# Kernel tuning notes

Hardware: AMD Instinct MI355X
Metric: run time of the kernel (lower is better)

Reference implementation:

```python
import jax, jax.numpy as jnp
import numpy as np

EPS = 1e-12
LAMBDA = 0.5  # kernel['lambda'] for the binary kernel

D, H, Z = 3072, 1024, 32
BS, NN = 128, 32


def setup_inputs() -> dict:
    key = jax.random.key(0)
    ks = jax.random.split(key, 16)
    sc = lambda fan_in: 1.0 / np.sqrt(fan_in)
    inp = {
        "x_c": jax.random.normal(ks[0], (BS, D), jnp.float32),
        "x_nn": jax.random.normal(ks[1], (BS, NN, D), jnp.float32),
        # encoder params: D -> H -> H -> Z
        "We1": jax.random.normal(ks[2], (D, H), jnp.float32) * sc(D),
        "be1": jnp.zeros((H,), jnp.float32),
        "We2": jax.random.normal(ks[3], (H, H), jnp.float32) * sc(H),
        "be2": jnp.zeros((H,), jnp.float32),
        "We3": jax.random.normal(ks[4], (H, Z), jnp.float32) * sc(H),
        "be3": jnp.zeros((Z,), jnp.float32),
        # decoder params: Z -> H -> H -> D
        "Wd1": jax.random.normal(ks[5], (Z, H), jnp.float32) * sc(Z),
        "bd1": jnp.zeros((H,), jnp.float32),
        "Wd2": jax.random.normal(ks[6], (H, H), jnp.float32) * sc(H),
        "bd2": jnp.zeros((H,), jnp.float32),
        "Wd3": jax.random.normal(ks[7], (H, D), jnp.float32) * sc(H),
        "bd3": jnp.zeros((D,), jnp.float32),
    }
    return inp


def _mlp(x, W1, b1, W2, b2, W3, b3):
    h = jax.nn.relu(x @ W1 + b1)
    h = jax.nn.relu(h @ W2 + b2)
    return h @ W3 + b3


def reference(x_c, x_nn, We1, be1, We2, be2, We3, be3,
              Wd1, bd1, Wd2, bd2, Wd3, bd3):
    bs, num_nn, dim = x_nn.shape

    enc = lambda x: _mlp(x, We1, be1, We2, be2, We3, be3)
    dec = lambda z: _mlp(z, Wd1, bd1, Wd2, bd2, Wd3, bd3)

    z_c = enc(x_c)                                   # (bs, Z)
    z_dim = z_c.shape[1]
    z_nn = enc(x_nn.reshape(-1, dim)).reshape(bs, num_nn, z_dim)

    recon = dec(z_c)                                 # (bs, D)
    dz = z_nn - z_c[:, None, :]                      # (bs, nn, Z)
    v = dz.reshape(-1, z_dim)                        # (bs*nn, Z)
    inputs = jnp.broadcast_to(z_c[:, None, :], (bs, num_nn, z_dim)).reshape(-1, z_dim)

    # approx_order == 2: Jacobian-vector and Hessian-bilinear (dz^T H dz) via nested jvp
    jac_fn = lambda z: jax.jvp(dec, (z,), (v,))[1]   # J(z) dz, (bs*nn, D)
    jac, hess = jax.jvp(jac_fn, (inputs,), (v,))     # each (bs*nn, D)

    n_recon = recon[:, None, :] + (jac + 0.5 * hess).reshape(bs, num_nn, dim)

    n_loss = jnp.sum((x_nn - n_recon) ** 2, axis=2)  # ||.||^2, (bs, nn)

    # binary kernel: 1 where neighbor differs from center, lambda where identical
    dist = jnp.linalg.norm(x_c[:, None, :] - x_nn, axis=2)
    weights = jnp.where(dist > EPS, 1.0, LAMBDA)

    loss = jnp.mean(weights * n_loss)
    return loss
```

## Files before the change

kernel.cpp:

```cpp
#include <hip/hip_runtime.h>
#include <math.h>

#define D_DIM 3072
#define H_DIM 1024
#define Z_DIM 32
#define BATCH 128
#define NNEI 32
#define NROWS (BATCH * NNEI)
#define MENC (NROWS + BATCH)

typedef __attribute__((ext_vector_type(8))) short short8;
typedef __attribute__((ext_vector_type(4))) float f32x4;
typedef unsigned short ushortT;

__device__ __forceinline__ unsigned short f2bf(float f) {
  union { float f; unsigned int u; } v; v.f = f;
  unsigned int r = v.u + 0x7FFFu + ((v.u >> 16) & 1u);
  return (unsigned short)(r >> 16);
}
__device__ __forceinline__ float bf2f(unsigned short b) {
  union { unsigned int u; float f; } v; v.u = ((unsigned int)b) << 16;
  return v.f;
}

enum { EP_RELU = 0, EP_BIAS = 1, EP_PART = 2, EP_LOSS = 3 };

template <int MODE, int TN>
__global__ __launch_bounds__(256) __attribute__((amdgpu_waves_per_eu(2, 4)))
void gemm64(
    const ushortT* __restrict__ A, const ushortT* __restrict__ BT,
    const float* __restrict__ bias, ushortT* __restrict__ C,
    float* __restrict__ P, int M, int N, int K, int Ks,
    const ushortT* __restrict__ xa,
    const float* __restrict__ wrow,
    float* __restrict__ out) {
  constexpr int NF = TN / 32;

  __shared__ __align__(16) ushortT As[8192];
  __shared__ __align__(16) ushortT Bs[TN * 64];

  const int t = threadIdx.x;
  const int wave = t >> 6;
  const int lane = t & 63;
  const int quad = lane >> 4;
  const int lm = lane & 15;

  int id = blockIdx.y * gridDim.x + blockIdx.x;
  const int nwg = gridDim.x * gridDim.y;
  if ((nwg & 7) == 0) id = (id & 7) * (nwg >> 3) + (id >> 3);
  const int bm = (id / gridDim.x) * 128;
  const int bn = (id % gridDim.x) * TN;

  const int koff = blockIdx.z * Ks;
  const int wr = (wave >> 1) * 64;
  const int wc = (wave & 1) * (TN / 2);

  f32x4 acc[4][NF];
#pragma unroll
  for (int i = 0; i < 4; ++i)
#pragma unroll
    for (int j = 0; j < NF; ++j) acc[i][j] = (f32x4)0.f;

  const int a_r0 = (t >> 6) * 16 + (t & 15);
  const int a_q8 = ((t >> 4) & 3) * 8;
  const ushortT* ga = A + (size_t)(bm + a_r0) * K + koff + a_q8;
  const size_t aK64 = (size_t)64 * K;

  const ushortT* gb = nullptr;
  if (TN >= 64) {
    gb = BT + (size_t)(bn + a_r0) * K + koff + a_q8;
  } else {
    const int b_r = ((t >> 6) & 1) * 16 + (t & 15);
    const int b_k = (t >> 7) * 32 + ((t >> 4) & 3) * 8;
    gb = BT + (size_t)(bn + b_r) * K + koff + b_k;
  }

  uint4 a0, a1, a2, a3, b0, b1 = {0,0,0,0}, b2 = {0,0,0,0}, b3 = {0,0,0,0};

#define LOADT(kk)                                               \
  {                                                             \
    const size_t o = (size_t)(kk) * 64;                         \
    a0 = *(const uint4*)(ga + o);                               \
    a1 = *(const uint4*)(ga + aK64 + o);                        \
    a2 = *(const uint4*)(ga + o + 32);                          \
    a3 = *(const uint4*)(ga + aK64 + o + 32);                   \
    b0 = *(const uint4*)(gb + o);                               \
    if (TN == 128) {                                            \
      b1 = *(const uint4*)(gb + aK64 + o);                      \
      b2 = *(const uint4*)(gb + o + 32);                        \
      b3 = *(const uint4*)(gb + aK64 + o + 32);                 \
    } else if (TN == 64) {                                      \
      b1 = *(const uint4*)(gb + o + 32);                        \
    }                                                           \
  }
#define STORET()                                                \
  {                                                             \
    *(uint4*)&As[t * 8] = a0;                                   \
    *(uint4*)&As[t * 8 + 2048] = a1;                            \
    *(uint4*)&As[t * 8 + 4096] = a2;                            \
    *(uint4*)&As[t * 8 + 6144] = a3;                            \
    *(uint4*)&Bs[t * 8] = b0;                                   \
    if (TN == 128) {                                            \
      *(uint4*)&Bs[t * 8 + 2048] = b1;                          \
      *(uint4*)&Bs[t * 8 + 4096] = b2;                          \
      *(uint4*)&Bs[t * 8 + 6144] = b3;                          \
    } else if (TN == 64) {                                      \
      *(uint4*)&Bs[t * 8 + 2048] = b1;                          \
    }                                                           \
  }

  const int nk = Ks / 64;
  LOADT(0);

  for (int k0 = 0; k0 < nk; ++k0) {
    __syncthreads();
    STORET();
    __syncthreads();
    if (k0 + 1 < nk) LOADT(k0 + 1);

#pragma unroll
    for (int kk = 0; kk < 2; ++kk) {
      const ushortT* arp = &As[kk * 4096 + (wr >> 4) * 512 + lane * 8];
      const ushortT* brp =
          &Bs[(TN == 128 ? kk * 4096 : TN == 64 ? kk * 2048 : kk * 1024) +
              (wc >> 4) * 512 + lane * 8];
      short8 af[4], bf[NF];
#pragma unroll
      for (int mt = 0; mt < 4; ++mt) af[mt] = *(const short8*)(arp + mt * 512);
#pragma unroll
      for (int nt = 0; nt < NF; ++nt) bf[nt] = *(const short8*)(brp + nt * 512);
#pragma unroll
      for (int mt = 0; mt < 4; ++mt)
#pragma unroll
        for (int nt = 0; nt < NF; ++nt)
          acc[mt][nt] = __builtin_amdgcn_mfma_f32_16x16x32_bf16(af[mt], bf[nt], acc[mt][nt], 0, 0, 0);
    }
  }
#undef LOADT
#undef STORET

  if (MODE == EP_LOSS) {
    __shared__ float red[256];
    float lsum = 0.f;
#pragma unroll
    for (int mt = 0; mt < 4; ++mt) {
#pragma unroll
      for (int r = 0; r < 4; ++r) {
        const int row = bm + wr + mt * 16 + quad * 4 + r;
        const float w = wrow[row];
        const ushortT* xr = xa + (size_t)row * N;
        float rs = 0.f;
#pragma unroll
        for (int nt = 0; nt < NF; ++nt) {
          const int col = bn + wc + nt * 16 + lm;
          const float d = bf2f(xr[col]) - (acc[mt][nt][r] + bias[col]);
          rs = fmaf(d, d, rs);
        }
        lsum = fmaf(w, rs, lsum);
      }
    }
    __syncthreads();
    red[t] = lsum;
    __syncthreads();
    for (int st = 128; st > 0; st >>= 1) {
      if (t < st) red[t] += red[t + st];
      __syncthreads();
    }
    if (t == 0) atomicAdd(out, red[0] * (1.0f / (float)NROWS));
  } else if (MODE == EP_PART) {
#pragma unroll
    for (int mt = 0; mt < 4; ++mt)
#pragma unroll
      for (int r = 0; r < 4; ++r) {
        const int row = bm + wr + mt * 16 + quad * 4 + r;
#pragma unroll
        for (int nt = 0; nt < NF; ++nt) {
          const int col = bn + wc + nt * 16 + lm;
          P[((size_t)blockIdx.z * M + row) * N + col] = acc[mt][nt][r];
        }
      }
  } else {
#pragma unroll
    for (int mt = 0; mt < 4; ++mt)
#pragma unroll
      for (int r = 0; r < 4; ++r) {
        const int row = bm + wr + mt * 16 + quad * 4 + r;
#pragma unroll
        for (int nt = 0; nt < NF; ++nt) {
          const int col = bn + wc + nt * 16 + lm;
          float v = acc[mt][nt][r] + bias[col];
          if (MODE == EP_RELU) v = fmaxf(v, 0.f);
          C[(size_t)row * N + col] = f2bf(v);
        }
      }
  }
}

template <int MODE, int TN>
__global__ __launch_bounds__(256) __attribute__((amdgpu_waves_per_eu(2, 4)))
void gemm_sb(
    const ushortT* __restrict__ A, const ushortT* __restrict__ BT,
    const float* __restrict__ bias, ushortT* __restrict__ C,
    int M, int N, int K,
    const ushortT* __restrict__ xa, const float* __restrict__ wrow,
    float* __restrict__ out) {
  constexpr int NF = TN / 32;
  __shared__ __align__(16) ushortT As[4096];
  __shared__ __align__(16) ushortT Bs[TN * 32];

  const int t = threadIdx.x;
  const int wave = t >> 6;
  const int lane = t & 63;
  const int quad = lane >> 4;
  const int lm = lane & 15;

  int id = blockIdx.y * gridDim.x + blockIdx.x;
  const int nwg = gridDim.x * gridDim.y;
  if ((nwg & 7) == 0) id = (id & 7) * (nwg >> 3) + (id >> 3);
  const int bm = (id / gridDim.x) * 128;
  const int bn = (id % gridDim.x) * TN;

  const int wr = (wave >> 1) * 64;
  const int wc = (wave & 1) * (TN / 2);

  f32x4 acc[4][NF];
#pragma unroll
  for (int i = 0; i < 4; ++i)
#pragma unroll
    for (int j = 0; j < NF; ++j) acc[i][j] = (f32x4)0.f;

  const int a_r0 = (t >> 6) * 16 + (t & 15);
  const int a_q8 = ((t >> 4) & 3) * 8;
  const ushortT* ga0 = A + (size_t)(bm + a_r0) * K + a_q8;
  const ushortT* ga1 = ga0 + (size_t)64 * K;
  const ushortT* gb0 = BT + (size_t)(bn + a_r0) * K + a_q8;
  const ushortT* gb1 = gb0 + (size_t)64 * K;

  uint4 ra0 = *(const uint4*)ga0;
  uint4 ra1 = *(const uint4*)ga1;
  uint4 rb0 = *(const uint4*)gb0;
  uint4 rb1 = {0, 0, 0, 0};
  if (TN == 128) rb1 = *(const uint4*)gb1;
  ga0 += 32; ga1 += 32; gb0 += 32; gb1 += 32;

  const ushortT* arp = As + (wr >> 4) * 512 + lane * 8;
  const ushortT* brp = Bs + (wc >> 4) * 512 + lane * 8;

  for (int k0 = 0; k0 < K; k0 += 32) {
    __syncthreads();
    *(uint4*)&As[t * 8] = ra0;
    *(uint4*)&As[t * 8 + 2048] = ra1;
    *(uint4*)&Bs[t * 8] = rb0;
    if (TN == 128) *(uint4*)&Bs[t * 8 + 2048] = rb1;
    __syncthreads();
    if (k0 + 32 < K) {
      ra0 = *(const uint4*)ga0;
      ra1 = *(const uint4*)ga1;
      rb0 = *(const uint4*)gb0;
      if (TN == 128) rb1 = *(const uint4*)gb1;
      ga0 += 32; ga1 += 32; gb0 += 32; gb1 += 32;
    }
    short8 af[4], bf[NF];
#pragma unroll
    for (int mt = 0; mt < 4; ++mt) af[mt] = *(const short8*)(arp + mt * 512);
#pragma unroll
    for (int nt = 0; nt < NF; ++nt) bf[nt] = *(const short8*)(brp + nt * 512);
#pragma unroll
    for (int mt = 0; mt < 4; ++mt)
#pragma unroll
      for (int nt = 0; nt < NF; ++nt)
        acc[mt][nt] = __builtin_amdgcn_mfma_f32_16x16x32_bf16(af[mt], bf[nt], acc[mt][nt], 0, 0, 0);
  }

#pragma unroll
  for (int mt = 0; mt < 4; ++mt)
#pragma unroll
    for (int r = 0; r < 4; ++r) {
      const int row = bm + wr + mt * 16 + quad * 4 + r;
#pragma unroll
      for (int nt = 0; nt < NF; ++nt) {
        const int col = bn + wc + nt * 16 + lm;
        float v = acc[mt][nt][r] + bias[col];
        if (MODE == EP_RELU) v = fmaxf(v, 0.f);
        C[(size_t)row * N + col] = f2bf(v);
      }
    }
}

template <int S>
__global__ __launch_bounds__(256) void reduce_lin(
    const float* __restrict__ P, const float* __restrict__ bias,
    ushortT* __restrict__ outp, int MN, int Nmask) {
  const int i4 = (blockIdx.x * 256 + threadIdx.x) * 4;
  if (i4 >= MN) return;
  float4 s = *(const float4*)(P + i4);
#pragma unroll
  for (int k = 1; k < S; ++k) {
    const float4 q = *(const float4*)(P + (size_t)k * MN + i4);
    s.x += q.x; s.y += q.y; s.z += q.z; s.w += q.w;
  }
  const float4 b = *(const float4*)(bias + (i4 & Nmask));
  ushort4 o;
  o.x = f2bf(s.x + b.x); o.y = f2bf(s.y + b.y);
  o.z = f2bf(s.z + b.z); o.w = f2bf(s.w + b.w);
  *(ushort4*)(outp + i4) = o;
}

__global__ __launch_bounds__(256) void mask_apply(
    const ushortT* __restrict__ U, ushortT* __restrict__ outp) {
  const int i4 = (blockIdx.x * 256 + threadIdx.x) * 4;
  const int r = i4 >> 10;
  const int c = i4 & 1023;
  ushort4 u = *(const ushort4*)(U + i4);
  ushort4 o;
  if (r < NROWS) {
    const ushort4 m = *(const ushort4*)(U + (((size_t)(NROWS + (r >> 5))) << 10) + c);
    o.x = ((short)m.x > 0) ? u.x : 0;
    o.y = ((short)m.y > 0) ? u.y : 0;
    o.z = ((short)m.z > 0) ? u.z : 0;
    o.w = ((short)m.w > 0) ? u.w : 0;
  } else {
    o.x = ((short)u.x > 0) ? u.x : 0;
    o.y = ((short)u.y > 0) ? u.y : 0;
    o.z = ((short)u.z > 0) ? u.z : 0;
    o.w = ((short)u.w > 0) ? u.w : 0;
  }
  *(ushort4*)(outp + i4) = o;
}

__global__ __launch_bounds__(256) void prep_kernel(
    const float* __restrict__ x_c, const float* __restrict__ x_nn,
    ushortT* __restrict__ A_enc, float* __restrict__ wbuf, float* __restrict__ out) {
  const int i = blockIdx.x;
  const int t = threadIdx.x;
  if (i < NROWS) {
    const float* src = x_nn + (size_t)i * D_DIM;
    const float* ctr = x_c + (size_t)(i >> 5) * D_DIM;
    ushortT* dst = A_enc + (size_t)i * D_DIM;
    float s = 0.f;
    for (int d = t * 4; d < D_DIM; d += 1024) {
      const float4 v = *(const float4*)(src + d);
      const float4 c = *(const float4*)(ctr + d);
      ushort4 o;
      o.x = f2bf(v.x); o.y = f2bf(v.y); o.z = f2bf(v.z); o.w = f2bf(v.w);
      *(ushort4*)(dst + d) = o;
      const float dx = v.x - c.x, dy = v.y - c.y, dz = v.z - c.z, dw = v.w - c.w;
      s += dx * dx + dy * dy + dz * dz + dw * dw;
    }
    __shared__ float red[256];
    red[t] = s;
    __syncthreads();
    for (int st = 128; st > 0; st >>= 1) {
      if (t < st) red[t] += red[t + st];
      __syncthreads();
    }
    if (t == 0) {
      wbuf[i] = (red[0] > 1e-24f) ? 1.0f : 0.5f;
      if (i == 0) out[0] = 0.f;
    }
  } else {
    const int r = i - NROWS;
    const float* src = x_c + (size_t)r * D_DIM;
    ushortT* dst = A_enc + (size_t)i * D_DIM;
    for (int d = t * 4; d < D_DIM; d += 1024) {
      const float4 v = *(const float4*)(src + d);
      ushort4 o;
      o.x = f2bf(v.x); o.y = f2bf(v.y); o.z = f2bf(v.z); o.w = f2bf(v.w);
      *(ushort4*)(dst + d) = o;
    }
  }
}

__global__ __launch_bounds__(256) void trans_all(
    const float* __restrict__ We1, const float* __restrict__ We2,
    const float* __restrict__ We3, const float* __restrict__ Wd1,
    const float* __restrict__ Wd2, const float* __restrict__ Wd3,
    ushortT* __restrict__ We1T, ushortT* __restrict__ We2T,
    ushortT* __restrict__ We3T, ushortT* __restrict__ Wd1T,
    ushortT* __restrict__ Wd2T, ushortT* __restrict__ Wd3T) {
  const int b = blockIdx.x;
  const float* W; ushortT* WT; int K, N, loc;
  if (b < 3072)      { W = We1; WT = We1T; K = 3072; N = 1024; loc = b; }
  else if (b < 4096) { W = We2; WT = We2T; K = 1024; N = 1024; loc = b - 3072; }
  else if (b < 4128) { W = We3; WT = We3T; K = 1024; N = 32;   loc = b - 4096; }
  else if (b < 4160) { W = Wd1; WT = Wd1T; K = 32;   N = 1024; loc = b - 4128; }
  else if (b < 5184) { W = Wd2; WT = Wd2T; K = 1024; N = 1024; loc = b - 4160; }
  else               { W = Wd3; WT = Wd3T; K = 1024; N = 3072; loc = b - 5184; }
  const int ntiles = N >> 5;
  const int n0 = (loc % ntiles) * 32;
  const int k0 = (loc / ntiles) * 32;
  __shared__ float tile[32][33];
  const int tx = threadIdx.x & 31;
  const int ty = threadIdx.x >> 5;
  for (int i = ty; i < 32; i += 8)
    tile[i][tx] = W[(size_t)(k0 + i) * N + n0 + tx];
  __syncthreads();
  for (int i = ty; i < 32; i += 8)
    WT[(size_t)(n0 + i) * K + k0 + tx] = f2bf(tile[tx][i]);
}

extern "C" void kernel_launch(void* const* d_in, const int* in_sizes, int n_in,
                              void* d_out, int out_size, void* d_ws, size_t ws_size,
                              hipStream_t stream) {
  const float* x_c = (const float*)d_in[0];
  const float* x_nn = (const float*)d_in[1];
  const float* We1 = (const float*)d_in[2];
  const float* be1 = (const float*)d_in[3];
  const float* We2 = (const float*)d_in[4];
  const float* be2 = (const float*)d_in[5];
  const float* We3 = (const float*)d_in[6];
  const float* be3 = (const float*)d_in[7];
  const float* Wd1 = (const float*)d_in[8];
  const float* bd1 = (const float*)d_in[9];
  const float* Wd2 = (const float*)d_in[10];
  const float* bd2 = (const float*)d_in[11];
  const float* Wd3 = (const float*)d_in[12];
  const float* bd3 = (const float*)d_in[13];
  float* out = (float*)d_out;

  char* p = (char*)d_ws;
  auto alloc = [&](size_t bytes) {
    char* r = p;
    p += (bytes + 255) & ~(size_t)255;
    return r;
  };
  ushortT* We1T = (ushortT*)alloc((size_t)H_DIM * D_DIM * 2);
  ushortT* We2T = (ushortT*)alloc((size_t)H_DIM * H_DIM * 2);
  ushortT* We3T = (ushortT*)alloc((size_t)Z_DIM * H_DIM * 2);
  ushortT* Wd1T = (ushortT*)alloc((size_t)H_DIM * Z_DIM * 2);
  ushortT* Wd2T = (ushortT*)alloc((size_t)H_DIM * H_DIM * 2);
  ushortT* Wd3T = (ushortT*)alloc((size_t)D_DIM * H_DIM * 2);
  ushortT* A_enc = (ushortT*)alloc((size_t)MENC * D_DIM * 2);
  ushortT* bufX = (ushortT*)alloc((size_t)MENC * H_DIM * 2);
  ushortT* bufY = (ushortT*)alloc((size_t)MENC * H_DIM * 2);
  ushortT* z = (ushortT*)alloc((size_t)MENC * Z_DIM * 2);
  float* Pz = (float*)alloc((size_t)8 * MENC * Z_DIM * 4);
  float* wbuf = (float*)alloc((size_t)NROWS * 4);

  const dim3 blk(256);
  const float* nofp = nullptr;
  const ushortT* nobf = nullptr;

  prep_kernel<<<dim3(MENC), blk, 0, stream>>>(x_c, x_nn, A_enc, wbuf, out);
  trans_all<<<dim3(8256), blk, 0, stream>>>(We1, We2, We3, Wd1, Wd2, Wd3,
                                            We1T, We2T, We3T, Wd1T, Wd2T, Wd3T);

  gemm64<EP_RELU, 64><<<dim3(16, 33, 1), blk, 0, stream>>>(
      A_enc, We1T, be1, bufX, nullptr, MENC, H_DIM, D_DIM, D_DIM, nobf, nofp, nullptr);
  gemm64<EP_RELU, 64><<<dim3(16, 33, 1), blk, 0, stream>>>(
      bufX, We2T, be2, bufY, nullptr, MENC, H_DIM, H_DIM, H_DIM, nobf, nofp, nullptr);
  gemm64<EP_PART, 32><<<dim3(1, 33, 8), blk, 0, stream>>>(
      bufY, We3T, nofp, nullptr, Pz, MENC, Z_DIM, H_DIM, H_DIM / 8, nobf, nofp, nullptr);
  reduce_lin<8><<<dim3((MENC * Z_DIM) / 1024), blk, 0, stream>>>(
      Pz, be3, z, MENC * Z_DIM, Z_DIM - 1);

  gemm_sb<EP_BIAS, 64><<<dim3(16, 33), blk, 0, stream>>>(
      z, Wd1T, bd1, bufX, MENC, H_DIM, Z_DIM, nobf, nofp, nullptr);
  mask_apply<<<dim3((MENC * H_DIM) / 1024), blk, 0, stream>>>(bufX, bufY);
  gemm64<EP_BIAS, 64><<<dim3(16, 33, 1), blk, 0, stream>>>(
      bufY, Wd2T, bd2, bufX, nullptr, MENC, H_DIM, H_DIM, H_DIM, nobf, nofp, nullptr);
  mask_apply<<<dim3((NROWS * H_DIM) / 1024), blk, 0, stream>>>(bufX, bufY);
  gemm64<EP_LOSS, 128><<<dim3(24, 32, 1), blk, 0, stream>>>(
      bufY, Wd3T, bd3, nullptr, nullptr, NROWS, D_DIM, H_DIM, H_DIM, A_enc, wbuf, out);
}
```

Measured before the change: 410.2 us.

## Double-buffer GEMM tiles via direct global-to-LDS loads and widen N tiles

Replaces the register-staged global-load-then-LDS-store scheme in the GEMM kernels with global_load_lds direct copies into double-buffered shared memory, using vmcnt waits and raw barriers so the next K tile streams in while the current one is computed. The single-K-step small GEMM is simplified to one direct load plus compute. The encoder and decoder hidden GEMMs move from 64-wide to 128-wide N tiles, halving the grid, and the waves_per_eu hint is dropped. This aims to cut VGPR staging and LDS store overhead and to improve latency hiding, at the cost of doubled LDS use, which may lower occupancy, and a smaller grid.

Result: faster. 401.6 us (-2.1%).

```diff
diff --git a/kernel.cpp b/kernel.cpp
--- a/kernel.cpp
+++ b/kernel.cpp
@@ -23,11 +23,27 @@
   return v.f;
 }
 
+__device__ __forceinline__ void gl16(const ushortT* g, ushortT* l) {
+  typedef __attribute__((address_space(1))) const void gvoid;
+  typedef __attribute__((address_space(3))) void lvoid;
+  __builtin_amdgcn_global_load_lds((gvoid*)(const void*)g, (lvoid*)(void*)l,
+                                   16, 0, 0);
+}
+
+template <int N>
+__device__ __forceinline__ void wait_vmcnt() {
+  if constexpr (N == 0)      asm volatile("s_waitcnt vmcnt(0)" ::: "memory");
+  else if constexpr (N == 5) asm volatile("s_waitcnt vmcnt(5)" ::: "memory");
+  else if constexpr (N == 6) asm volatile("s_waitcnt vmcnt(6)" ::: "memory");
+  else if constexpr (N == 8) asm volatile("s_waitcnt vmcnt(8)" ::: "memory");
+}
+#define BAR() asm volatile("s_barrier" ::: "memory")
+#define LGKM0() asm volatile("s_waitcnt lgkmcnt(0)" ::: "memory")
+
 enum { EP_RELU = 0, EP_BIAS = 1, EP_PART = 2, EP_LOSS = 3 };
 
 template <int MODE, int TN>
-__global__ __launch_bounds__(256) __attribute__((amdgpu_waves_per_eu(2, 4)))
-void gemm64(
+__global__ __launch_bounds__(256) void gemm64(
     const ushortT* __restrict__ A, const ushortT* __restrict__ BT,
     const float* __restrict__ bias, ushortT* __restrict__ C,
     float* __restrict__ P, int M, int N, int K, int Ks,
@@ -35,9 +51,10 @@
     const float* __restrict__ wrow,
     float* __restrict__ out) {
   constexpr int NF = TN / 32;
-
-  __shared__ __align__(16) ushortT As[8192];
-  __shared__ __align__(16) ushortT Bs[TN * 64];
+  constexpr int NLD = 4 + NF;
+
+  __shared__ __align__(16) ushortT As[2][8192];
+  __shared__ __align__(16) ushortT Bs[2][TN * 64];
 
   const int t = threadIdx.x;
   const int wave = t >> 6;
@@ -66,7 +83,7 @@
   const ushortT* ga = A + (size_t)(bm + a_r0) * K + koff + a_q8;
   const size_t aK64 = (size_t)64 * K;
 
-  const ushortT* gb = nullptr;
+  const ushortT* gb;
   if (TN >= 64) {
     gb = BT + (size_t)(bn + a_r0) * K + koff + a_q8;
   } else {
@@ -75,69 +92,81 @@
     gb = BT + (size_t)(bn + b_r) * K + koff + b_k;
   }
 
-  uint4 a0, a1, a2, a3, b0, b1 = {0,0,0,0}, b2 = {0,0,0,0}, b3 = {0,0,0,0};
-
-#define LOADT(kk)                                               \
+  ushortT* asw0 = &As[0][wave * 512];
+  ushortT* asw1 = &As[1][wave * 512];
+  ushortT* bsw0 = &Bs[0][wave * 512];
+  ushortT* bsw1 = &Bs[1][wave * 512];
+
+#define STAGE(asw, bsw, kk)                                     \
   {                                                             \
     const size_t o = (size_t)(kk) * 64;                         \
-    a0 = *(const uint4*)(ga + o);                               \
-    a1 = *(const uint4*)(ga + aK64 + o);                        \
-    a2 = *(const uint4*)(ga + o + 32);                          \
-    a3 = *(const uint4*)(ga + aK64 + o + 32);                   \
-    b0 = *(const uint4*)(gb + o);                               \
+    gl16(ga + o, (asw));                                        \
+    gl16(ga + aK64 + o, (asw) + 2048);                          \
+    gl16(ga + o + 32, (asw) + 4096);                            \
+    gl16(ga + aK64 + o + 32, (asw) + 6144);                     \
+    gl16(gb + o, (bsw));                                        \
     if (TN == 128) {                                            \
-      b1 = *(const uint4*)(gb + aK64 + o);                      \
-      b2 = *(const uint4*)(gb + o + 32);                        \
-      b3 = *(const uint4*)(gb + aK64 + o + 32);                 \
+      gl16(gb + aK64 + o, (bsw) + 2048);                        \
+      gl16(gb + o + 32, (bsw) + 4096);                          \
+      gl16(gb + aK64 + o + 32, (bsw) + 6144);                   \
     } else if (TN == 64) {                                      \
-      b1 = *(const uint4*)(gb + o + 32);                        \
+      gl16(gb + o + 32, (bsw) + 2048);                          \
     }                                                           \
   }
-#define STORET()                                                \
-  {                                                             \
-    *(uint4*)&As[t * 8] = a0;                                   \
-    *(uint4*)&As[t * 8 + 2048] = a1;                            \
-    *(uint4*)&As[t * 8 + 4096] = a2;                            \
-    *(uint4*)&As[t * 8 + 6144] = a3;                            \
-    *(uint4*)&Bs[t * 8] = b0;                                   \
-    if (TN == 128) {                                            \
-      *(uint4*)&Bs[t * 8 + 2048] = b1;                          \
-      *(uint4*)&Bs[t * 8 + 4096] = b2;                          \
-      *(uint4*)&Bs[t * 8 + 6144] = b3;                          \
-    } else if (TN == 64) {                                      \
-      *(uint4*)&Bs[t * 8 + 2048] = b1;                          \
-    }                                                           \
+
+#define COMPUTE(b)                                                            \
+  {                                                                           \
+    _Pragma("unroll")                                                         \
+    for (int kk = 0; kk < 2; ++kk) {                                          \
+      const ushortT* arp = &As[b][kk * 4096 + (wr >> 4) * 512 + lane * 8];    \
+      const ushortT* brp =                                                    \
+          &Bs[b][(TN == 128 ? kk * 4096 : TN == 64 ? kk * 2048 : kk * 1024) + \
+                 (wc >> 4) * 512 + lane * 8];                                 \
+      short8 af[4], bf[NF];                                                   \
+      _Pragma("unroll")                                                       \
+      for (int mt = 0; mt < 4; ++mt)                                          \
+        af[mt] = *(const short8*)(arp + mt * 512);                            \
+      _Pragma("unroll")                                                       \
+      for (int nt = 0; nt < NF; ++nt)                                         \
+        bf[nt] = *(const short8*)(brp + nt * 512);                            \
+      _Pragma("unroll")                                                       \
+      for (int mt = 0; mt < 4; ++mt)                                          \
+        _Pragma("unroll")                                                     \
+        for (int nt = 0; nt < NF; ++nt)                                       \
+          acc[mt][nt] = __builtin_amdgcn_mfma_f32_16x16x32_bf16(              \
+              af[mt], bf[nt], acc[mt][nt], 0, 0, 0);                          \
+    }                                                                         \
   }
 
   const int nk = Ks / 64;
-  LOADT(0);
-
-  for (int k0 = 0; k0 < nk; ++k0) {
-    __syncthreads();
-    STORET();
-    __syncthreads();
-    if (k0 + 1 < nk) LOADT(k0 + 1);
-
-#pragma unroll
-    for (int kk = 0; kk < 2; ++kk) {
-      const ushortT* arp = &As[kk * 4096 + (wr >> 4) * 512 + lane * 8];
-      const ushortT* brp =
-          &Bs[(TN == 128 ? kk * 4096 : TN == 64 ? kk * 2048 : kk * 1024) +
-              (wc >> 4) * 512 + lane * 8];
-      short8 af[4], bf[NF];
-#pragma unroll
-      for (int mt = 0; mt < 4; ++mt) af[mt] = *(const short8*)(arp + mt * 512);
-#pragma unroll
-      for (int nt = 0; nt < NF; ++nt) bf[nt] = *(const short8*)(brp + nt * 512);
-#pragma unroll
-      for (int mt = 0; mt < 4; ++mt)
-#pragma unroll
-        for (int nt = 0; nt < NF; ++nt)
-          acc[mt][nt] = __builtin_amdgcn_mfma_f32_16x16x32_bf16(af[mt], bf[nt], acc[mt][nt], 0, 0, 0);
-    }
-  }
-#undef LOADT
-#undef STORET
+  STAGE(asw0, bsw0, 0);
+
+  for (int k0 = 0; k0 < nk; k0 += 2) {
+    BAR();
+    if (k0 + 1 < nk) {
+      STAGE(asw1, bsw1, k0 + 1);
+      wait_vmcnt<NLD>();
+    } else {
+      wait_vmcnt<0>();
+    }
+    BAR();
+    COMPUTE(0);
+    LGKM0();
+    if (k0 + 1 < nk) {
+      BAR();
+      if (k0 + 2 < nk) {
+        STAGE(asw0, bsw0, k0 + 2);
+        wait_vmcnt<NLD>();
+      } else {
+        wait_vmcnt<0>();
+      }
+      BAR();
+      COMPUTE(1);
+      LGKM0();
+    }
+  }
+#undef STAGE
+#undef COMPUTE
 
   if (MODE == EP_LOSS) {
     __shared__ float red[256];
@@ -197,8 +226,7 @@
 }
 
 template <int MODE, int TN>
-__global__ __launch_bounds__(256) __attribute__((amdgpu_waves_per_eu(2, 4)))
-void gemm_sb(
+__global__ __launch_bounds__(256) void gemm_sb(
     const ushortT* __restrict__ A, const ushortT* __restrict__ BT,
     const float* __restrict__ bias, ushortT* __restrict__ C,
     int M, int N, int K,
@@ -223,54 +251,39 @@
   const int wr = (wave >> 1) * 64;
   const int wc = (wave & 1) * (TN / 2);
 
-  f32x4 acc[4][NF];
-#pragma unroll
-  for (int i = 0; i < 4; ++i)
-#pragma unroll
-    for (int j = 0; j < NF; ++j) acc[i][j] = (f32x4)0.f;
-
   const int a_r0 = (t >> 6) * 16 + (t & 15);
   const int a_q8 = ((t >> 4) & 3) * 8;
   const ushortT* ga0 = A + (size_t)(bm + a_r0) * K + a_q8;
-  const ushortT* ga1 = ga0 + (size_t)64 * K;
   const ushortT* gb0 = BT + (size_t)(bn + a_r0) * K + a_q8;
-  const ushortT* gb1 = gb0 + (size_t)64 * K;
-
-  uint4 ra0 = *(const uint4*)ga0;
-  uint4 ra1 = *(const uint4*)ga1;
-  uint4 rb0 = *(const uint4*)gb0;
-  uint4 rb1 = {0, 0, 0, 0};
-  if (TN == 128) rb1 = *(const uint4*)gb1;
-  ga0 += 32; ga1 += 32; gb0 += 32; gb1 += 32;
+
+  ushortT* asw = &As[wave * 512];
+  ushortT* bsw = &Bs[wave * 512];
+  gl16(ga0, asw);
+  gl16(ga0 + (size_t)64 * K, asw + 2048);
+  gl16(gb0, bsw);
+  if (TN == 128) gl16(gb0 + (size_t)64 * K, bsw + 2048);
+  wait_vmcnt<0>();
+  BAR();
+
+  f32x4 acc[4][NF];
+#pragma unroll
+  for (int i = 0; i < 4; ++i)
+#pragma unroll
+    for (int j = 0; j < NF; ++j) acc[i][j] = (f32x4)0.f;
 
   const ushortT* arp = As + (wr >> 4) * 512 + lane * 8;
   const ushortT* brp = Bs + (wc >> 4) * 512 + lane * 8;
-
-  for (int k0 = 0; k0 < K; k0 += 32) {
-    __syncthreads();
-    *(uint4*)&As[t * 8] = ra0;
-    *(uint4*)&As[t * 8 + 2048] = ra1;
-    *(uint4*)&Bs[t * 8] = rb0;
-    if (TN == 128) *(uint4*)&Bs[t * 8 + 2048] = rb1;
-    __syncthreads();
-    if (k0 + 32 < K) {
-      ra0 = *(const uint4*)ga0;
-      ra1 = *(const uint4*)ga1;
-      rb0 = *(const uint4*)gb0;
-      if (TN == 128) rb1 = *(const uint4*)gb1;
-      ga0 += 32; ga1 += 32; gb0 += 32; gb1 += 32;
-    }
-    short8 af[4], bf[NF];
-#pragma unroll
-    for (int mt = 0; mt < 4; ++mt) af[mt] = *(const short8*)(arp + mt * 512);
-#pragma unroll
-    for (int nt = 0; nt < NF; ++nt) bf[nt] = *(const short8*)(brp + nt * 512);
-#pragma unroll
-    for (int mt = 0; mt < 4; ++mt)
-#pragma unroll
-      for (int nt = 0; nt < NF; ++nt)
-        acc[mt][nt] = __builtin_amdgcn_mfma_f32_16x16x32_bf16(af[mt], bf[nt], acc[mt][nt], 0, 0, 0);
-  }
+  short8 af[4], bf[NF];
+#pragma unroll
+  for (int mt = 0; mt < 4; ++mt) af[mt] = *(const short8*)(arp + mt * 512);
+#pragma unroll
+  for (int nt = 0; nt < NF; ++nt) bf[nt] = *(const short8*)(brp + nt * 512);
+#pragma unroll
+  for (int mt = 0; mt < 4; ++mt)
+#pragma unroll
+    for (int nt = 0; nt < NF; ++nt)
+      acc[mt][nt] = __builtin_amdgcn_mfma_f32_16x16x32_bf16(
+          af[mt], bf[nt], acc[mt][nt], 0, 0, 0);
 
 #pragma unroll
   for (int mt = 0; mt < 4; ++mt)
@@ -445,9 +458,9 @@
   trans_all<<<dim3(8256), blk, 0, stream>>>(We1, We2, We3, Wd1, Wd2, Wd3,
                                             We1T, We2T, We3T, Wd1T, Wd2T, Wd3T);
 
-  gemm64<EP_RELU, 64><<<dim3(16, 33, 1), blk, 0, stream>>>(
+  gemm64<EP_RELU, 128><<<dim3(8, 33, 1), blk, 0, stream>>>(
       A_enc, We1T, be1, bufX, nullptr, MENC, H_DIM, D_DIM, D_DIM, nobf, nofp, nullptr);
-  gemm64<EP_RELU, 64><<<dim3(16, 33, 1), blk, 0, stream>>>(
+  gemm64<EP_RELU, 128><<<dim3(8, 33, 1), blk, 0, stream>>>(
       bufX, We2T, be2, bufY, nullptr, MENC, H_DIM, H_DIM, H_DIM, nobf, nofp, nullptr);
   gemm64<EP_PART, 32><<<dim3(1, 33, 8), blk, 0, stream>>>(
       bufY, We3T, nofp, nullptr, Pz, MENC, Z_DIM, H_DIM, H_DIM / 8, nobf, nofp, nullptr);
@@ -457,7 +470,7 @@
   gemm_sb<EP_BIAS, 64><<<dim3(16, 33), blk, 0, stream>>>(
       z, Wd1T, bd1, bufX, MENC, H_DIM, Z_DIM, nobf, nofp, nullptr);
   mask_apply<<<dim3((MENC * H_DIM) / 1024), blk, 0, stream>>>(bufX, bufY);
-  gemm64<EP_BIAS, 64><<<dim3(16, 33, 1), blk, 0, stream>>>(
+  gemm64<EP_BIAS, 128><<<dim3(8, 33, 1), blk, 0, stream>>>(
       bufY, Wd2T, bd2, bufX, nullptr, MENC, H_DIM, H_DIM, H_DIM, nobf, nofp, nullptr);
   mask_apply<<<dim3((NROWS * H_DIM) / 1024), blk, 0, stream>>>(bufX, bufY);
   gemm64<EP_LOSS, 128><<<dim3(24, 32, 1), blk, 0, stream>>>(
```

## Use direct global-to-LDS loads, K32 tiles, and split-K with reduce for hidden GEMMs

Applied to the files above, without the earlier changes.

Replaces the register-staged GEMM main loop with global_load_lds direct-to-LDS copies using 32-wide K tiles, and drops the register prefetch. The hidden-layer GEMMs switch to 128-wide N tiles with split-K partial sums in fp32, followed by a reduce kernel that now also applies bias and ReLU. The aim is to cut VGPR staging cost and raise occupancy and parallelism. In exchange, each K step is no longer overlapped with the next load, and the split-K partials add extra fp32 traffic and extra kernel launches.

Result: faster. 381.1 us (-7.1%).

```diff
diff --git a/kernel.cpp b/kernel.cpp
--- a/kernel.cpp
+++ b/kernel.cpp
@@ -23,11 +23,20 @@
   return v.f;
 }
 
+__device__ __forceinline__ void gl16(const ushortT* g, ushortT* l) {
+  typedef __attribute__((address_space(1))) const void gvoid;
+  typedef __attribute__((address_space(3))) void lvoid;
+  __builtin_amdgcn_global_load_lds((gvoid*)(const void*)g, (lvoid*)(void*)l,
+                                   16, 0, 0);
+}
+#define BAR() asm volatile("s_barrier" ::: "memory")
+#define VM0() asm volatile("s_waitcnt vmcnt(0)" ::: "memory")
+
 enum { EP_RELU = 0, EP_BIAS = 1, EP_PART = 2, EP_LOSS = 3 };
 
 template <int MODE, int TN>
-__global__ __launch_bounds__(256) __attribute__((amdgpu_waves_per_eu(2, 4)))
-void gemm64(
+__global__ __launch_bounds__(256) __attribute__((amdgpu_waves_per_eu(3)))
+void gemm32(
     const ushortT* __restrict__ A, const ushortT* __restrict__ BT,
     const float* __restrict__ bias, ushortT* __restrict__ C,
     float* __restrict__ P, int M, int N, int K, int Ks,
@@ -36,8 +45,8 @@
     float* __restrict__ out) {
   constexpr int NF = TN / 32;
 
-  __shared__ __align__(16) ushortT As[8192];
-  __shared__ __align__(16) ushortT Bs[TN * 64];
+  __shared__ __align__(16) ushortT As[4096];
+  __shared__ __align__(16) ushortT Bs[TN * 32];
 
   const int t = threadIdx.x;
   const int wave = t >> 6;
@@ -61,83 +70,54 @@
 #pragma unroll
     for (int j = 0; j < NF; ++j) acc[i][j] = (f32x4)0.f;
 
-  const int a_r0 = (t >> 6) * 16 + (t & 15);
-  const int a_q8 = ((t >> 4) & 3) * 8;
-  const ushortT* ga = A + (size_t)(bm + a_r0) * K + koff + a_q8;
-  const size_t aK64 = (size_t)64 * K;
-
-  const ushortT* gb = nullptr;
-  if (TN >= 64) {
-    gb = BT + (size_t)(bn + a_r0) * K + koff + a_q8;
+  const int srow = lane & 15;
+  const int skq = lane >> 4;
+  const ushortT* gA =
+      A + (size_t)(bm + wave * 32 + srow) * K + koff + skq * 8;
+  const size_t row16 = (size_t)16 * K;
+
+  const ushortT* gB;
+  if (TN == 128) {
+    gB = BT + (size_t)(bn + wave * 32 + srow) * K + koff + skq * 8;
+  } else if (TN == 64) {
+    gB = BT + (size_t)(bn + wave * 16 + srow) * K + koff + skq * 8;
   } else {
-    const int b_r = ((t >> 6) & 1) * 16 + (t & 15);
-    const int b_k = (t >> 7) * 32 + ((t >> 4) & 3) * 8;
-    gb = BT + (size_t)(bn + b_r) * K + koff + b_k;
-  }
-
-  uint4 a0, a1, a2, a3, b0, b1 = {0,0,0,0}, b2 = {0,0,0,0}, b3 = {0,0,0,0};
-
-#define LOADT(kk)                                               \
-  {                                                             \
-    const size_t o = (size_t)(kk) * 64;                         \
-    a0 = *(const uint4*)(ga + o);                               \
-    a1 = *(const uint4*)(ga + aK64 + o);                        \
-    a2 = *(const uint4*)(ga + o + 32);                          \
-    a3 = *(const uint4*)(ga + aK64 + o + 32);                   \
-    b0 = *(const uint4*)(gb + o);                               \
-    if (TN == 128) {                                            \
-      b1 = *(const uint4*)(gb + aK64 + o);                      \
-      b2 = *(const uint4*)(gb + o + 32);                        \
-      b3 = *(const uint4*)(gb + aK64 + o + 32);                 \
-    } else if (TN == 64) {                                      \
-      b1 = *(const uint4*)(gb + o + 32);                        \
-    }                                                           \
-  }
-#define STORET()                                                \
-  {                                                             \
-    *(uint4*)&As[t * 8] = a0;                                   \
-    *(uint4*)&As[t * 8 + 2048] = a1;                            \
-    *(uint4*)&As[t * 8 + 4096] = a2;                            \
-    *(uint4*)&As[t * 8 + 6144] = a3;                            \
-    *(uint4*)&Bs[t * 8] = b0;                                   \
-    if (TN == 128) {                                            \
-      *(uint4*)&Bs[t * 8 + 2048] = b1;                          \
-      *(uint4*)&Bs[t * 8 + 4096] = b2;                          \
-      *(uint4*)&Bs[t * 8 + 6144] = b3;                          \
-    } else if (TN == 64) {                                      \
-      *(uint4*)&Bs[t * 8 + 2048] = b1;                          \
-    }                                                           \
-  }
-
-  const int nk = Ks / 64;
-  LOADT(0);
-
+    gB = BT + (size_t)(bn + (wave & 1) * 16 + srow) * K + koff + skq * 8;
+  }
+
+  ushortT* lA = &As[wave * 1024];
+  ushortT* lB = (TN == 128) ? &Bs[wave * 1024] : &Bs[(wave & 1) * 512];
+
+  const int nk = Ks / 32;
   for (int k0 = 0; k0 < nk; ++k0) {
     __syncthreads();
-    STORET();
+    const size_t o = (size_t)k0 * 32;
+    gl16(gA + o, lA);
+    gl16(gA + row16 + o, lA + 512);
+    if (TN == 128) {
+      gl16(gB + o, lB);
+      gl16(gB + row16 + o, lB + 512);
+    } else if (TN == 64) {
+      gl16(gB + o, lB);
+    } else {
+      if (wave < 2) gl16(gB + o, lB);
+    }
     __syncthreads();
-    if (k0 + 1 < nk) LOADT(k0 + 1);
-
-#pragma unroll
-    for (int kk = 0; kk < 2; ++kk) {
-      const ushortT* arp = &As[kk * 4096 + (wr >> 4) * 512 + lane * 8];
-      const ushortT* brp =
-          &Bs[(TN == 128 ? kk * 4096 : TN == 64 ? kk * 2048 : kk * 1024) +
-              (wc >> 4) * 512 + lane * 8];
-      short8 af[4], bf[NF];
-#pragma unroll
-      for (int mt = 0; mt < 4; ++mt) af[mt] = *(const short8*)(arp + mt * 512);
-#pragma unroll
-      for (int nt = 0; nt < NF; ++nt) bf[nt] = *(const short8*)(brp + nt * 512);
-#pragma unroll
-      for (int mt = 0; mt < 4; ++mt)
-#pragma unroll
-        for (int nt = 0; nt < NF; ++nt)
-          acc[mt][nt] = __builtin_amdgcn_mfma_f32_16x16x32_bf16(af[mt], bf[nt], acc[mt][nt], 0, 0, 0);
-    }
-  }
-#undef LOADT
-#undef STORET
+
+    const ushortT* arp = &As[(wr >> 4) * 512 + lane * 8];
+    const ushortT* brp = &Bs[(wc >> 4) * 512 + lane * 8];
+    short8 af[4], bf[NF];
+#pragma unroll
+    for (int mt = 0; mt < 4; ++mt) af[mt] = *(const short8*)(arp + mt * 512);
+#pragma unroll
+    for (int nt = 0; nt < NF; ++nt) bf[nt] = *(const short8*)(brp + nt * 512);
+#pragma unroll
+    for (int mt = 0; mt < 4; ++mt)
+#pragma unroll
+      for (int nt = 0; nt < NF; ++nt)
+        acc[mt][nt] = __builtin_amdgcn_mfma_f32_16x16x32_bf16(
+            af[mt], bf[nt], acc[mt][nt], 0, 0, 0);
+  }
 
   if (MODE == EP_LOSS) {
     __shared__ float red[256];
@@ -197,8 +177,7 @@
 }
 
 template <int MODE, int TN>
-__global__ __launch_bounds__(256) __attribute__((amdgpu_waves_per_eu(2, 4)))
-void gemm_sb(
+__global__ __launch_bounds__(256) void gemm_sb(
     const ushortT* __restrict__ A, const ushortT* __restrict__ BT,
     const float* __restrict__ bias, ushortT* __restrict__ C,
     int M, int N, int K,
@@ -223,54 +202,39 @@
   const int wr = (wave >> 1) * 64;
   const int wc = (wave & 1) * (TN / 2);
 
-  f32x4 acc[4][NF];
-#pragma unroll
-  for (int i = 0; i < 4; ++i)
-#pragma unroll
-    for (int j = 0; j < NF; ++j) acc[i][j] = (f32x4)0.f;
-
   const int a_r0 = (t >> 6) * 16 + (t & 15);
   const int a_q8 = ((t >> 4) & 3) * 8;
   const ushortT* ga0 = A + (size_t)(bm + a_r0) * K + a_q8;
-  const ushortT* ga1 = ga0 + (size_t)64 * K;
   const ushortT* gb0 = BT + (size_t)(bn + a_r0) * K + a_q8;
-  const ushortT* gb1 = gb0 + (size_t)64 * K;
-
-  uint4 ra0 = *(const uint4*)ga0;
-  uint4 ra1 = *(const uint4*)ga1;
-  uint4 rb0 = *(const uint4*)gb0;
-  uint4 rb1 = {0, 0, 0, 0};
-  if (TN == 128) rb1 = *(const uint4*)gb1;
-  ga0 += 32; ga1 += 32; gb0 += 32; gb1 += 32;
+
+  ushortT* asw = &As[wave * 512];
+  ushortT* bsw = &Bs[wave * 512];
+  gl16(ga0, asw);
+  gl16(ga0 + (size_t)64 * K, asw + 2048);
+  gl16(gb0, bsw);
+  if (TN == 128) gl16(gb0 + (size_t)64 * K, bsw + 2048);
+  VM0();
+  BAR();
+
+  f32x4 acc[4][NF];
+#pragma unroll
+  for (int i = 0; i < 4; ++i)
+#pragma unroll
+    for (int j = 0; j < NF; ++j) acc[i][j] = (f32x4)0.f;
 
   const ushortT* arp = As + (wr >> 4) * 512 + lane * 8;
   const ushortT* brp = Bs + (wc >> 4) * 512 + lane * 8;
-
-  for (int k0 = 0; k0 < K; k0 += 32) {
-    __syncthreads();
-    *(uint4*)&As[t * 8] = ra0;
-    *(uint4*)&As[t * 8 + 2048] = ra1;
-    *(uint4*)&Bs[t * 8] = rb0;
-    if (TN == 128) *(uint4*)&Bs[t * 8 + 2048] = rb1;
-    __syncthreads();
-    if (k0 + 32 < K) {
-      ra0 = *(const uint4*)ga0;
-      ra1 = *(const uint4*)ga1;
-      rb0 = *(const uint4*)gb0;
-      if (TN == 128) rb1 = *(const uint4*)gb1;
-      ga0 += 32; ga1 += 32; gb0 += 32; gb1 += 32;
-    }
-    short8 af[4], bf[NF];
-#pragma unroll
-    for (int mt = 0; mt < 4; ++mt) af[mt] = *(const short8*)(arp + mt * 512);
-#pragma unroll
-    for (int nt = 0; nt < NF; ++nt) bf[nt] = *(const short8*)(brp + nt * 512);
-#pragma unroll
-    for (int mt = 0; mt < 4; ++mt)
-#pragma unroll
-      for (int nt = 0; nt < NF; ++nt)
-        acc[mt][nt] = __builtin_amdgcn_mfma_f32_16x16x32_bf16(af[mt], bf[nt], acc[mt][nt], 0, 0, 0);
-  }
+  short8 af[4], bf[NF];
+#pragma unroll
+  for (int mt = 0; mt < 4; ++mt) af[mt] = *(const short8*)(arp + mt * 512);
+#pragma unroll
+  for (int nt = 0; nt < NF; ++nt) bf[nt] = *(const short8*)(brp + nt * 512);
+#pragma unroll
+  for (int mt = 0; mt < 4; ++mt)
+#pragma unroll
+    for (int nt = 0; nt < NF; ++nt)
+      acc[mt][nt] = __builtin_amdgcn_mfma_f32_16x16x32_bf16(
+          af[mt], bf[nt], acc[mt][nt], 0, 0, 0);
 
 #pragma unroll
   for (int mt = 0; mt < 4; ++mt)
@@ -287,7 +251,7 @@
     }
 }
 
-template <int S>
+template <int S, int RELU>
 __global__ __launch_bounds__(256) void reduce_lin(
     const float* __restrict__ P, const float* __restrict__ bias,
     ushortT* __restrict__ outp, int MN, int Nmask) {
@@ -300,9 +264,13 @@
     s.x += q.x; s.y += q.y; s.z += q.z; s.w += q.w;
   }
   const float4 b = *(const float4*)(bias + (i4 & Nmask));
+  float vx = s.x + b.x, vy = s.y + b.y, vz = s.z + b.z, vw = s.w + b.w;
+  if (RELU) {
+    vx = fmaxf(vx, 0.f); vy = fmaxf(vy, 0.f);
+    vz = fmaxf(vz, 0.f); vw = fmaxf(vw, 0.f);
+  }
   ushort4 o;
-  o.x = f2bf(s.x + b.x); o.y = f2bf(s.y + b.y);
-  o.z = f2bf(s.z + b.z); o.w = f2bf(s.w + b.w);
+  o.x = f2bf(vx); o.y = f2bf(vy); o.z = f2bf(vz); o.w = f2bf(vw);
   *(ushort4*)(outp + i4) = o;
 }
 
@@ -434,7 +402,7 @@
   ushortT* bufX = (ushortT*)alloc((size_t)MENC * H_DIM * 2);
   ushortT* bufY = (ushortT*)alloc((size_t)MENC * H_DIM * 2);
   ushortT* z = (ushortT*)alloc((size_t)MENC * Z_DIM * 2);
-  float* Pz = (float*)alloc((size_t)8 * MENC * Z_DIM * 4);
+  float* Pbig = (float*)alloc((size_t)3 * MENC * H_DIM * 4);
   float* wbuf = (float*)alloc((size_t)NROWS * 4);
 
   const dim3 blk(256);
@@ -445,21 +413,34 @@
   trans_all<<<dim3(8256), blk, 0, stream>>>(We1, We2, We3, Wd1, Wd2, Wd3,
                                             We1T, We2T, We3T, Wd1T, Wd2T, Wd3T);
 
-  gemm64<EP_RELU, 64><<<dim3(16, 33, 1), blk, 0, stream>>>(
-      A_enc, We1T, be1, bufX, nullptr, MENC, H_DIM, D_DIM, D_DIM, nobf, nofp, nullptr);
-  gemm64<EP_RELU, 64><<<dim3(16, 33, 1), blk, 0, stream>>>(
-      bufX, We2T, be2, bufY, nullptr, MENC, H_DIM, H_DIM, H_DIM, nobf, nofp, nullptr);
-  gemm64<EP_PART, 32><<<dim3(1, 33, 8), blk, 0, stream>>>(
-      bufY, We3T, nofp, nullptr, Pz, MENC, Z_DIM, H_DIM, H_DIM / 8, nobf, nofp, nullptr);
-  reduce_lin<8><<<dim3((MENC * Z_DIM) / 1024), blk, 0, stream>>>(
-      Pz, be3, z, MENC * Z_DIM, Z_DIM - 1);
+  gemm32<EP_PART, 128><<<dim3(8, 33, 3), blk, 0, stream>>>(
+      A_enc, We1T, nofp, nullptr, Pbig, MENC, H_DIM, D_DIM, D_DIM / 3,
+      nobf, nofp, nullptr);
+  reduce_lin<3, 1><<<dim3((MENC * H_DIM) / 1024), blk, 0, stream>>>(
+      Pbig, be1, bufX, MENC * H_DIM, H_DIM - 1);
+
+  gemm32<EP_PART, 128><<<dim3(8, 33, 2), blk, 0, stream>>>(
+      bufX, We2T, nofp, nullptr, Pbig, MENC, H_DIM, H_DIM, H_DIM / 2,
+      nobf, nofp, nullptr);
+  reduce_lin<2, 1><<<dim3((MENC * H_DIM) / 1024), blk, 0, stream>>>(
+      Pbig, be2, bufY, MENC * H_DIM, H_DIM - 1);
+
+  gemm32<EP_PART, 32><<<dim3(1, 33, 8), blk, 0, stream>>>(
+      bufY, We3T, nofp, nullptr, Pbig, MENC, Z_DIM, H_DIM, H_DIM / 8,
+      nobf, nofp, nullptr);
+  reduce_lin<8, 0><<<dim3((MENC * Z_DIM) / 1024), blk, 0, stream>>>(
+      Pbig, be3, z, MENC * Z_DIM, Z_DIM - 1);
 
   gemm_sb<EP_BIAS, 64><<<dim3(16, 33), blk, 0, stream>>>(
       z, Wd1T, bd1, bufX, MENC, H_DIM, Z_DIM, nobf, nofp, nullptr);
   mask_apply<<<dim3((MENC * H_DIM) / 1024), blk, 0, stream>>>(bufX, bufY);
-  gemm64<EP_BIAS, 64><<<dim3(16, 33, 1), blk, 0, stream>>>(
-      bufY, Wd2T, bd2, bufX, nullptr, MENC, H_DIM, H_DIM, H_DIM, nobf, nofp, nullptr);
+  gemm32<EP_PART, 128><<<dim3(8, 33, 2), blk, 0, stream>>>(
+      bufY, Wd2T, nofp, nullptr, Pbig, MENC, H_DIM, H_DIM, H_DIM / 2,
+      nobf, nofp, nullptr);
+  reduce_lin<2, 0><<<dim3((MENC * H_DIM) / 1024), blk, 0, stream>>>(
+      Pbig, bd2, bufX, MENC * H_DIM, H_DIM - 1);
   mask_apply<<<dim3((NROWS * H_DIM) / 1024), blk, 0, stream>>>(bufX, bufY);
-  gemm64<EP_LOSS, 128><<<dim3(24, 32, 1), blk, 0, stream>>>(
-      bufY, Wd3T, bd3, nullptr, nullptr, NROWS, D_DIM, H_DIM, H_DIM, A_enc, wbuf, out);
-}
+  gemm32<EP_LOSS, 128><<<dim3(24, 32, 1), blk, 0, stream>>>(
+      bufY, Wd3T, bd3, nullptr, nullptr, NROWS, D_DIM, H_DIM, H_DIM,
+      A_enc, wbuf, out);
+}
```
